# Kernel tuning notes

Hardware: AMD Instinct MI355X
Metric: run time of the kernel (lower is better)

## Reference

```python
import jax, jax.numpy as jnp
import numpy as np

N, D, C = 131072, 256, 1000
EPS = 1e-6


def setup_inputs() -> dict:
    key = jax.random.key(0)
    k1, k2, k3, k4 = jax.random.split(key, 4)
    feats = jax.random.normal(k1, (N, D), dtype=jnp.float32)
    pseudo_lbls = jax.random.randint(k2, (N,), 0, C)
    src_proto = jax.random.normal(k3, (C, D), dtype=jnp.float32)
    # uniform in [0.5, 1.5) to keep the Mahalanobis denominator well-conditioned
    src_proto_cov = jax.random.uniform(k4, (C, D), dtype=jnp.float32) + 0.5
    return {"feats": feats, "pseudo_lbls": pseudo_lbls,
            "src_proto": src_proto, "src_proto_cov": src_proto_cov}


def reference(feats, pseudo_lbls, src_proto, src_proto_cov):
    # Fused scatter-mean over classes (replaces the python loop over unique labels).
    num_classes, feat_dim = src_proto.shape
    counts = jax.ops.segment_sum(jnp.ones((feats.shape[0],), feats.dtype),
                                 pseudo_lbls, num_segments=num_classes)  # [C]
    sums = jax.ops.segment_sum(feats, pseudo_lbls, num_segments=num_classes)  # [C, D]
    means = sums / jnp.maximum(counts, 1.0)[:, None]                      # [C, D]
    present = counts > 0                                                  # [C]
    # GSSLoss: mean over the [n_uniq, D] elements of (mean - proto)^2 / (cov + eps)
    per_elem = (means - src_proto) ** 2 / (src_proto_cov + EPS)           # [C, D]
    per_elem = jnp.where(present[:, None], per_elem, 0.0)
    n_present = jnp.sum(present.astype(feats.dtype))
    loss = jnp.sum(per_elem) / (n_present * feat_dim)
    return loss
```

## Files before the change

### kernel.cpp

```cpp
#include <hip/hip_runtime.h>

#define EPS 1e-6f
#define MAX_C 1000
#define W 32
#define NCHUNKS 32
#define T 64
#define RPC 4096
#define SBLK 1024


__global__ __launch_bounds__(256)
void hist_kernel(const int* __restrict__ lbls, int* __restrict__ counts,
                 int n, int c_total) {
    __shared__ int h[MAX_C];
    for (int i = threadIdx.x; i < c_total; i += 256) h[i] = 0;
    __syncthreads();
    int tid = blockIdx.x * 256 + threadIdx.x;
    int n4 = n >> 2;
    const int4* l4 = (const int4*)lbls;
    for (int i = tid; i < n4; i += gridDim.x * 256) {
        int4 v = l4[i];
        atomicAdd(&h[v.x], 1); atomicAdd(&h[v.y], 1);
        atomicAdd(&h[v.z], 1); atomicAdd(&h[v.w], 1);
    }
    if (tid == 0)
        for (int i = n4 << 2; i < n; ++i) atomicAdd(&counts[lbls[i]], 1);
    __syncthreads();
    for (int i = threadIdx.x; i < c_total; i += 256)
        if (h[i] > 0) atomicAdd(&counts[i], h[i]);
}

__global__ __launch_bounds__(SBLK)
void stream_kernel(const float* __restrict__ feats,
                   const int* __restrict__ lbls,
                   float* __restrict__ partials,
                   int n, int d, int nslices, int c_total) {
    int slice = blockIdx.x % nslices;
    int chunk = blockIdx.x / nslices;
    int t    = threadIdx.x;
    int w    = t >> 6;
    int lane = t & 63;
    int half = lane >> 5;
    int col  = lane & 31;

    __shared__ float acc[MAX_C * W];
    __shared__ float stage[T * W];
    __shared__ int   lbl_s[RPC];

    int cW = c_total * W;
    for (int i = t; i < cW; i += SBLK) acc[i] = 0.0f;

    int base = chunk * RPC;
    int rows = RPC; if (base + rows > n) rows = n - base;

    for (int i = t; i < rows; i += SBLK) lbl_s[i] = lbls[base + i];

    const float* fbase = feats + (size_t)base * d + slice * W;
    int srow = t >> 3, sc = t & 7;
    bool stager = (t < T * 8);

    float4 ld = make_float4(0.f, 0.f, 0.f, 0.f);
    if (stager && srow < rows)
        ld = *(const float4*)(fbase + (size_t)srow * d + sc * 4);
    __syncthreads();
    if (stager) *(float4*)&stage[srow * W + sc * 4] = ld;
    __syncthreads();

    int ntiles = (rows + T - 1) / T;
    for (int tile = 0; tile < ntiles; ++tile) {
        int nrow0 = (tile + 1) * T;
        if (stager && nrow0 + srow < rows)
            ld = *(const float4*)(fbase + (size_t)(nrow0 + srow) * d + sc * 4);

        int r0 = tile * T;
        int rloc = r0 + lane;
        int lab = (rloc < rows) ? lbl_s[rloc] : -1;
        bool mine = (lab >= 0) && ((lab & 15) == w);
        unsigned long long mask = __ballot(mine);
        while (mask) {
            int rA = (int)__ffsll((unsigned long long)mask) - 1; mask &= mask - 1;
            int rB = -1;
            if (mask) { rB = (int)__ffsll((unsigned long long)mask) - 1; mask &= mask - 1; }
            int lA = __shfl(lab, rA);
            int lB = (rB >= 0) ? __shfl(lab, rB) : -1;
            int rAl = rA - r0 + r0;
            if (rB >= 0 && lA == lB) {
                if (half == 0) {
                    float v = stage[rA * W + col] + stage[rB * W + col];
                    acc[lA * W + col] += v;
                }
            } else {
                int r = half ? rB : rA;
                int l = half ? lB : lA;
                if (r >= 0)
                    acc[l * W + col] += stage[r * W + col];
            }
            (void)rAl;
        }
        __syncthreads();
        if (tile + 1 < ntiles && stager)
            *(float4*)&stage[srow * W + sc * 4] = ld;
        __syncthreads();
    }

    float* pbase = partials + (size_t)chunk * c_total * d + slice * W;
    for (int i = t; i < cW; i += SBLK) {
        int cls = i >> 5;
        int cc  = i & (W - 1);
        pbase[(size_t)cls * d + cc] = acc[i];
    }
}

__global__ __launch_bounds__(256)
void finalize_kernel(const float* __restrict__ partials,
                     const int* __restrict__ counts,
                     const float* __restrict__ proto,
                     const float* __restrict__ cov,
                     float* __restrict__ loss_acc,
                     float* __restrict__ npres_acc,
                     int* __restrict__ done,
                     float* __restrict__ out, int c_total, int d, int nchunks) {
    int c = blockIdx.x;
    int t = threadIdx.x;
    size_t idx = (size_t)c * d + t;
    size_t cstride = (size_t)c_total * d;

    float a = 0.0f;
    for (int k = 0; k < nchunks; ++k)
        a += partials[(size_t)k * cstride + idx];

    int cnt = counts[c];
    float present = (cnt > 0) ? 1.0f : 0.0f;
    float mean = a / fmaxf((float)cnt, 1.0f);
    float diff = mean - proto[idx];
    float pe = present * diff * diff / (cov[idx] + EPS);

    for (int off = 32; off > 0; off >>= 1)
        pe += __shfl_down(pe, off, 64);
    __shared__ float s[4];
    if ((t & 63) == 0) s[t >> 6] = pe;
    __syncthreads();
    if (t == 0) {
        atomicAdd(loss_acc, (s[0] + s[1]) + (s[2] + s[3]));
        atomicAdd(npres_acc, present);
        __threadfence();
        int prev = atomicAdd(done, 1);
        if (prev == c_total - 1) {
            float L = atomicAdd(loss_acc, 0.0f);
            float P = atomicAdd(npres_acc, 0.0f);
            out[0] = L / (P * (float)d);
        }
    }
}

extern "C" void kernel_launch(void* const* d_in, const int* in_sizes, int n_in,
                              void* d_out, int out_size, void* d_ws, size_t ws_size,
                              hipStream_t stream) {
    const float* feats = (const float*)d_in[0];
    const int*   lbls  = (const int*)d_in[1];
    const float* proto = (const float*)d_in[2];
    const float* cov   = (const float*)d_in[3];

    int n_rows = in_sizes[1];
    int d      = in_sizes[0] / n_rows;
    int c      = in_sizes[2] / d;

    int*   counts    = (int*)d_ws;
    float* loss_acc  = (float*)d_ws + c;
    float* npres_acc = loss_acc + 1;
    int*   done      = (int*)d_ws + c + 2;
    float* partials  = (float*)d_ws + c + 3;

    hipMemsetAsync(d_ws, 0, ((size_t)c + 3) * sizeof(int), stream);

    hist_kernel<<<128, 256, 0, stream>>>(lbls, counts, n_rows, c);

    int nslices = d / W;
    stream_kernel<<<nslices * NCHUNKS, SBLK, 0, stream>>>(
        feats, lbls, partials, n_rows, d, nslices, c);
    finalize_kernel<<<c, 256, 0, stream>>>(partials, counts, proto, cov,
                                           loss_acc, npres_acc, done,
                                           (float*)d_out, c, d, NCHUNKS);
}
```

Before: 291.6 us.

## Fuse label histogram into stream kernel and batch 256-row tiles with 4-way merge

Removes the separate histogram kernel by having the slice-0 blocks of the stream kernel count labels in shared memory. Row tiles grow from 64 to 256 rows, staged two float4 per thread, with labels double-buffered per tile instead of preloaded for the whole chunk. The scatter loop now handles eight rows per iteration: each half-wave merges up to four rows with equal labels, then merges across halves via shuffles, so fewer read-modify-writes hit the shared accumulator. In exchange there is more register pressure and branching, and the slice-0 blocks do extra histogram work.

```diff
diff --git a/kernel.cpp b/kernel.cpp
--- a/kernel.cpp
+++ b/kernel.cpp
@@ -3,37 +3,16 @@
 #define EPS 1e-6f
 #define MAX_C 1000
 #define W 32
-#define NCHUNKS 32
-#define T 64
+#define TR 256
 #define RPC 4096
 #define SBLK 1024
 
-
-__global__ __launch_bounds__(256)
-void hist_kernel(const int* __restrict__ lbls, int* __restrict__ counts,
-                 int n, int c_total) {
-    __shared__ int h[MAX_C];
-    for (int i = threadIdx.x; i < c_total; i += 256) h[i] = 0;
-    __syncthreads();
-    int tid = blockIdx.x * 256 + threadIdx.x;
-    int n4 = n >> 2;
-    const int4* l4 = (const int4*)lbls;
-    for (int i = tid; i < n4; i += gridDim.x * 256) {
-        int4 v = l4[i];
-        atomicAdd(&h[v.x], 1); atomicAdd(&h[v.y], 1);
-        atomicAdd(&h[v.z], 1); atomicAdd(&h[v.w], 1);
-    }
-    if (tid == 0)
-        for (int i = n4 << 2; i < n; ++i) atomicAdd(&counts[lbls[i]], 1);
-    __syncthreads();
-    for (int i = threadIdx.x; i < c_total; i += 256)
-        if (h[i] > 0) atomicAdd(&counts[i], h[i]);
-}
 
 __global__ __launch_bounds__(SBLK)
 void stream_kernel(const float* __restrict__ feats,
                    const int* __restrict__ lbls,
                    float* __restrict__ partials,
+                   int* __restrict__ counts,
                    int n, int d, int nslices, int c_total) {
     int slice = blockIdx.x % nslices;
     int chunk = blockIdx.x / nslices;
@@ -44,62 +23,134 @@
     int col  = lane & 31;
 
     __shared__ float acc[MAX_C * W];
-    __shared__ float stage[T * W];
-    __shared__ int   lbl_s[RPC];
+    __shared__ __align__(16) float stage[TR * W];
+    __shared__ int lbl_t[TR];
 
     int cW = c_total * W;
-    for (int i = t; i < cW; i += SBLK) acc[i] = 0.0f;
-
     int base = chunk * RPC;
     int rows = RPC; if (base + rows > n) rows = n - base;
-
-    for (int i = t; i < rows; i += SBLK) lbl_s[i] = lbls[base + i];
+    int ntiles = (rows + TR - 1) / TR;
 
     const float* fbase = feats + (size_t)base * d + slice * W;
-    int srow = t >> 3, sc = t & 7;
-    bool stager = (t < T * 8);
-
-    float4 ld = make_float4(0.f, 0.f, 0.f, 0.f);
-    if (stager && srow < rows)
-        ld = *(const float4*)(fbase + (size_t)srow * d + sc * 4);
+    int sr0 = t >> 3;
+    int sr1 = sr0 + 128;
+    int sc4 = t & 7;
+
+    float4 p0 = make_float4(0.f, 0.f, 0.f, 0.f), p1 = p0;
+    int plab = -1;
+    if (sr0 < rows) p0 = *(const float4*)(fbase + (size_t)sr0 * d + sc4 * 4);
+    if (sr1 < rows) p1 = *(const float4*)(fbase + (size_t)sr1 * d + sc4 * 4);
+    if (t < TR) plab = (t < rows) ? lbls[base + t] : -1;
+
+    for (int i = t; i < cW; i += SBLK) acc[i] = 0.0f;
+
+    if (slice == 0) {
+        int* hist = (int*)stage;
+        for (int i = t; i < c_total; i += SBLK) hist[i] = 0;
+        __syncthreads();
+        for (int i = t; i < rows; i += SBLK) atomicAdd(&hist[lbls[base + i]], 1);
+        __syncthreads();
+        for (int i = t; i < c_total; i += SBLK) {
+            int h = hist[i];
+            if (h) atomicAdd(&counts[i], h);
+        }
+    }
     __syncthreads();
-    if (stager) *(float4*)&stage[srow * W + sc * 4] = ld;
+
+    if (t < TR) lbl_t[t] = plab;
+    *(float4*)&stage[sr0 * W + sc4 * 4] = p0;
+    *(float4*)&stage[sr1 * W + sc4 * 4] = p1;
     __syncthreads();
 
-    int ntiles = (rows + T - 1) / T;
     for (int tile = 0; tile < ntiles; ++tile) {
-        int nrow0 = (tile + 1) * T;
-        if (stager && nrow0 + srow < rows)
-            ld = *(const float4*)(fbase + (size_t)(nrow0 + srow) * d + sc * 4);
-
-        int r0 = tile * T;
-        int rloc = r0 + lane;
-        int lab = (rloc < rows) ? lbl_s[rloc] : -1;
-        bool mine = (lab >= 0) && ((lab & 15) == w);
-        unsigned long long mask = __ballot(mine);
-        while (mask) {
-            int rA = (int)__ffsll((unsigned long long)mask) - 1; mask &= mask - 1;
-            int rB = -1;
-            if (mask) { rB = (int)__ffsll((unsigned long long)mask) - 1; mask &= mask - 1; }
-            int lA = __shfl(lab, rA);
-            int lB = (rB >= 0) ? __shfl(lab, rB) : -1;
-            int rAl = rA - r0 + r0;
-            if (rB >= 0 && lA == lB) {
-                if (half == 0) {
-                    float v = stage[rA * W + col] + stage[rB * W + col];
-                    acc[lA * W + col] += v;
-                }
+        if (tile + 1 < ntiles) {
+            int nb = (tile + 1) * TR;
+            p0 = make_float4(0.f, 0.f, 0.f, 0.f); p1 = p0; plab = -1;
+            int r0g = nb + sr0, r1g = nb + sr1;
+            if (r0g < rows) p0 = *(const float4*)(fbase + (size_t)r0g * d + sc4 * 4);
+            if (r1g < rows) p1 = *(const float4*)(fbase + (size_t)r1g * d + sc4 * 4);
+            if (t < TR) plab = (nb + t < rows) ? lbls[base + nb + t] : -1;
+        }
+
+        int l0 = lbl_t[lane];
+        int l1 = lbl_t[lane + 64];
+        int l2 = lbl_t[lane + 128];
+        int l3 = lbl_t[lane + 192];
+        unsigned long long m0 = __ballot(l0 >= 0 && (l0 & 15) == w);
+        unsigned long long m1 = __ballot(l1 >= 0 && (l1 & 15) == w);
+        unsigned long long m2 = __ballot(l2 >= 0 && (l2 & 15) == w);
+        unsigned long long m3 = __ballot(l3 >= 0 && (l3 & 15) == w);
+
+        unsigned long long cur = m0; int mi = 0;
+        auto nxt = [&]() -> int {
+            for (;;) {
+                if (cur) { int b = __ffsll(cur) - 1; cur &= cur - 1; return (mi << 6) + b; }
+                if (mi == 3) return -1;
+                ++mi;
+                cur = (mi == 1) ? m1 : (mi == 2) ? m2 : m3;
+            }
+        };
+
+        for (;;) {
+            int b0 = nxt(); if (b0 < 0) break;
+            int b1 = nxt(), b2 = nxt(), b3 = nxt();
+            int b4 = nxt(), b5 = nxt(), b6 = nxt(), b7 = nxt();
+
+            int ra = half ? b4 : b0, rb = half ? b5 : b1;
+            int rc = half ? b6 : b2, rd = half ? b7 : b3;
+            bool va = ra >= 0, vb = rb >= 0, vc = rc >= 0, vd = rd >= 0;
+            int la  = va ? lbl_t[ra] : -1;
+            int lb  = vb ? lbl_t[rb] : -1;
+            int lc  = vc ? lbl_t[rc] : -1;
+            int ld_ = vd ? lbl_t[rd] : -1;
+            float sa  = va ? stage[ra * W + col] : 0.f;
+            float sb  = vb ? stage[rb * W + col] : 0.f;
+            float sc_ = vc ? stage[rc * W + col] : 0.f;
+            float sd  = vd ? stage[rd * W + col] : 0.f;
+
+            if (vb && lb == la) { sa += sb; vb = false; }
+            if (vc && lc == la) { sa += sc_; vc = false; }
+            else if (vc && vb && lc == lb) { sb += sc_; vc = false; }
+            if (vd && ld_ == la) { sa += sd; vd = false; }
+            else if (vd && vb && ld_ == lb) { sb += sd; vd = false; }
+            else if (vd && vc && ld_ == lc) { sc_ += sd; vd = false; }
+
+            int ola  = __shfl_xor(la, 32),  olb  = __shfl_xor(lb, 32);
+            int olc  = __shfl_xor(lc, 32),  old_ = __shfl_xor(ld_, 32);
+            float osa = __shfl_xor(sa, 32), osb = __shfl_xor(sb, 32);
+            float osc = __shfl_xor(sc_, 32), osd = __shfl_xor(sd, 32);
+            int met  = (va ? 1 : 0) | (vb ? 2 : 0) | (vc ? 4 : 0) | (vd ? 8 : 0);
+            int omet = __shfl_xor(met, 32);
+            bool oa = (omet & 1), ob = (omet & 2), oc = (omet & 4), od = (omet & 8);
+            if (half == 0) {
+                if (oa) { if (va && ola == la) sa += osa; else if (vb && ola == lb) sb += osa; else if (vc && ola == lc) sc_ += osa; else if (vd && ola == ld_) sd += osa; }
+                if (ob) { if (va && olb == la) sa += osb; else if (vb && olb == lb) sb += osb; else if (vc && olb == lc) sc_ += osb; else if (vd && olb == ld_) sd += osb; }
+                if (oc) { if (va && olc == la) sa += osc; else if (vb && olc == lb) sb += osc; else if (vc && olc == lc) sc_ += osc; else if (vd && olc == ld_) sd += osc; }
+                if (od) { if (va && old_ == la) sa += osd; else if (vb && old_ == lb) sb += osd; else if (vc && old_ == lc) sc_ += osd; else if (vd && old_ == ld_) sd += osd; }
             } else {
-                int r = half ? rB : rA;
-                int l = half ? lB : lA;
-                if (r >= 0)
-                    acc[l * W + col] += stage[r * W + col];
+                if (va && ((oa && ola == la) || (ob && olb == la) || (oc && olc == la) || (od && old_ == la))) va = false;
+                if (vb && ((oa && ola == lb) || (ob && olb == lb) || (oc && olc == lb) || (od && old_ == lb))) vb = false;
+                if (vc && ((oa && ola == lc) || (ob && olb == lc) || (oc && olc == lc) || (od && old_ == lc))) vc = false;
+                if (vd && ((oa && ola == ld_) || (ob && olb == ld_) || (oc && olc == ld_) || (od && old_ == ld_))) vd = false;
             }
-            (void)rAl;
-        }
-        __syncthreads();
-        if (tile + 1 < ntiles && stager)
-            *(float4*)&stage[srow * W + sc * 4] = ld;
+
+            float xa = 0.f, xb = 0.f, xc = 0.f, xd = 0.f;
+            if (va) xa = acc[la * W + col];
+            if (vb) xb = acc[lb * W + col];
+            if (vc) xc = acc[lc * W + col];
+            if (vd) xd = acc[ld_ * W + col];
+            if (va) acc[la * W + col] = xa + sa;
+            if (vb) acc[lb * W + col] = xb + sb;
+            if (vc) acc[lc * W + col] = xc + sc_;
+            if (vd) acc[ld_ * W + col] = xd + sd;
+        }
+
+        __syncthreads();
+        if (tile + 1 < ntiles) {
+            if (t < TR) lbl_t[t] = plab;
+            *(float4*)&stage[sr0 * W + sc4 * 4] = p0;
+            *(float4*)&stage[sr1 * W + sc4 * 4] = p1;
+        }
         __syncthreads();
     }
 
@@ -173,12 +224,11 @@
 
     hipMemsetAsync(d_ws, 0, ((size_t)c + 3) * sizeof(int), stream);
 
-    hist_kernel<<<128, 256, 0, stream>>>(lbls, counts, n_rows, c);
-
     int nslices = d / W;
-    stream_kernel<<<nslices * NCHUNKS, SBLK, 0, stream>>>(
-        feats, lbls, partials, n_rows, d, nslices, c);
+    int nchunks = (n_rows + RPC - 1) / RPC;
+    stream_kernel<<<nslices * nchunks, SBLK, 0, stream>>>(
+        feats, lbls, partials, counts, n_rows, d, nslices, c);
     finalize_kernel<<<c, 256, 0, stream>>>(partials, counts, proto, cov,
                                            loss_acc, npres_acc, done,
-                                           (float*)d_out, c, d, NCHUNKS);
+                                           (float*)d_out, c, d, nchunks);
 }
```

Result: slower. 341.3 us (+17.1%).
